# Kernel optimization log

Measured on AMD Instinct MI355X. Metric: run time of the kernel, lower is better.

The kernel has to match this reference:

```python
import jax, jax.numpy as jnp
import numpy as np

B, S, D, H = 2, 2048, 1024, 16
HD = D // H


def setup_inputs() -> dict:
    key = jax.random.key(0)
    ks = jax.random.split(key, 6)
    std = 1.0 / np.sqrt(D)
    return {
        "hidden_states": jax.random.normal(ks[0], (B, S, D), dtype=jnp.float32),
        "attention_mask": jnp.zeros((B, 1, S, S), dtype=jnp.float32),
        "Wq": jax.random.normal(ks[1], (D, D), dtype=jnp.float32) * std,
        "bq": jnp.zeros((D,), dtype=jnp.float32),
        "Wk": jax.random.normal(ks[2], (D, D), dtype=jnp.float32) * std,
        "bk": jnp.zeros((D,), dtype=jnp.float32),
        "Wv": jax.random.normal(ks[3], (D, D), dtype=jnp.float32) * std,
        "bv": jnp.zeros((D,), dtype=jnp.float32),
        "Wo": jax.random.normal(ks[4], (D, D), dtype=jnp.float32) * std,
        "bo": jnp.zeros((D,), dtype=jnp.float32),
    }


def reference(hidden_states, attention_mask, Wq, bq, Wk, bk, Wv, bv, Wo, bo):
    scale = HD ** (-0.5)
    # torch Linear: y = x @ W^T + b
    def proj(x, W, b):
        y = jnp.einsum('bsd,ed->bse', x, W) + b
        return y.reshape(B, S, H, HD).transpose(0, 2, 1, 3)  # [B,H,S,HD]
    q = proj(hidden_states, Wq, bq)
    k = proj(hidden_states, Wk, bk)
    v = proj(hidden_states, Wv, bv)
    scores = jnp.einsum('bhqd,bhkd->bhqk', q, k) * scale + attention_mask
    attn = jax.nn.softmax(scores, axis=-1)  # dropout p=0.0 -> identity
    out = jnp.einsum('bhqk,bhkd->bhqd', attn, v)
    out = out.transpose(0, 2, 1, 3).reshape(B, S, D)
    return jnp.einsum('bsd,ed->bse', out, Wo) + bo
```

## Files before the change

### kernel.cpp

```cpp
#include <hip/hip_runtime.h>
#include <hip/hip_bf16.h>
#include <stdint.h>

#define Bb 2
#define Ss 2048
#define Dd 1024
#define Hh 16
#define HD 64

typedef __attribute__((ext_vector_type(8))) __bf16 bf16x8;
typedef __attribute__((ext_vector_type(4))) __bf16 bf16x4;
typedef __attribute__((ext_vector_type(2))) __bf16 bf16x2;
typedef __attribute__((ext_vector_type(4))) float f32x4;
typedef __attribute__((ext_vector_type(16))) float f32x16;

#define LOG2E 1.44269504088896f
#define SCL2 (0.125f * LOG2E)

#define HS_N   (Bb * Ss * Dd)
#define W_N    (Dd * Dd)
#define B_N    (Dd)
#define CAN_HS 0
#define CAN_WQ (CAN_HS + HS_N)
#define CAN_BQ (CAN_WQ + W_N)
#define CAN_WK (CAN_BQ + B_N)
#define CAN_BK (CAN_WK + W_N)
#define CAN_WV (CAN_BK + B_N)
#define CAN_BV (CAN_WV + W_N)
#define CAN_WO (CAN_BV + B_N)
#define CAN_BO (CAN_WO + W_N)
#define CAN_END (CAN_BO + B_N)
#define TSZ    (Bb * Hh * Ss * HD)
#define WS_ELEMS (CAN_END + 4 * TSZ)
#define WS_NEED ((size_t)WS_ELEMS * 2)

__device__ __forceinline__ void gl_lds16(const __bf16* g, __bf16* l) {
  __builtin_amdgcn_global_load_lds(
      (const __attribute__((address_space(1))) void*)g,
      (__attribute__((address_space(3))) void*)l,
      16, 0, 0);
}

__device__ __forceinline__ void gl_lds16f(const float* g, float* l) {
  __builtin_amdgcn_global_load_lds(
      (const __attribute__((address_space(1))) void*)g,
      (__attribute__((address_space(3))) void*)l,
      16, 0, 0);
}

__device__ __forceinline__ void cfence() { asm volatile("" ::: "memory"); }

__global__ void canon_kernel(const float* hs, const float* Wq, const float* bq,
                             const float* Wk, const float* bk, const float* Wv,
                             const float* bv, const float* Wo, const float* bo,
                             __bf16* __restrict__ dst) {
  const float* srcs[9] = {hs, Wq, bq, Wk, bk, Wv, bv, Wo, bo};
  const long starts[10] = {CAN_HS, CAN_WQ, CAN_BQ, CAN_WK, CAN_BK,
                           CAN_WV, CAN_BV, CAN_WO, CAN_BO, CAN_END};
  const long nchunks = CAN_END / 8;
  for (long c = blockIdx.x * blockDim.x + threadIdx.x; c < nchunks;
       c += (long)gridDim.x * blockDim.x) {
    const long i = c * 8;
    int seg = 0;
#pragma unroll
    for (int t = 1; t < 9; t++) seg += (i >= starts[t]) ? 1 : 0;
    const float* s = srcs[seg] + (i - starts[seg]);
    bf16x8 v;
#pragma unroll
    for (int e = 0; e < 8; e++) v[e] = (__bf16)s[e];
    *(bf16x8*)(dst + i) = v;
  }
}

template <int MODE, typename OutT>
__global__ __launch_bounds__(256, 2) void gemm_bt(
    const __bf16* __restrict__ A,
    const __bf16* __restrict__ W0, const __bf16* __restrict__ W1,
    const __bf16* __restrict__ W2,
    const __bf16* __restrict__ b0, const __bf16* __restrict__ b1,
    const __bf16* __restrict__ b2,
    OutT* __restrict__ O0, OutT* __restrict__ O1, OutT* __restrict__ O2) {
  __shared__ __align__(16) __bf16 sA[128 * 32 + 12544];
  __shared__ __align__(16) __bf16 sB[128 * 32];
  const int tid = threadIdx.x;
  const int lane = tid & 63;
  const int wid = tid >> 6;
  const int quad = lane >> 4;
  const int l15 = lane & 15;
  const int mBlock = blockIdx.x * 128;

  const __bf16* W;
  const __bf16* bias;
  OutT* Out;
  int nBlock, which = 0;
  if (MODE == 0) {
    which = blockIdx.y >> 3;
    nBlock = (blockIdx.y & 7) * 128;
    W = which == 0 ? W0 : (which == 1 ? W1 : W2);
    bias = which == 0 ? b0 : (which == 1 ? b1 : b2);
    Out = which == 0 ? O0 : (which == 1 ? O1 : O2);
  } else {
    nBlock = blockIdx.y * 128;
    W = W0;
    bias = b0;
    Out = O0;
  }

  const int waveM = (wid >> 1) * 64;
  const int waveN = (wid & 1) * 64;

  f32x4 acc[4][4] = {};

  const int c1 = wid * 64 + lane;
  const int c2 = c1 + 256;
  const __bf16* Ar1 = A + (mBlock + (c1 >> 2)) * Dd + (c1 & 3) * 8;
  const __bf16* Ar2 = A + (mBlock + (c2 >> 2)) * Dd + (c2 & 3) * 8;
  const __bf16* Wr1 = W + (nBlock + (c1 >> 2)) * Dd + (c1 & 3) * 8;
  const __bf16* Wr2 = W + (nBlock + (c2 >> 2)) * Dd + (c2 & 3) * 8;
  __bf16* ldsA1 = sA + (wid * 64) * 8;
  __bf16* ldsA2 = sA + (wid * 64 + 256) * 8;
  __bf16* ldsB1 = sB + (wid * 64) * 8;
  __bf16* ldsB2 = sB + (wid * 64 + 256) * 8;

  for (int k0 = 0; k0 < Dd; k0 += 32) {
    gl_lds16(Ar1 + k0, ldsA1);
    gl_lds16(Ar2 + k0, ldsA2);
    gl_lds16(Wr1 + k0, ldsB1);
    gl_lds16(Wr2 + k0, ldsB2);
    __syncthreads();

    bf16x8 aF[4], bF[4];
#pragma unroll
    for (int mi = 0; mi < 4; mi++)
      aF[mi] = *(const bf16x8*)(sA + (waveM + mi * 16 + l15) * 32 + quad * 8);
#pragma unroll
    for (int ni = 0; ni < 4; ni++)
      bF[ni] = *(const bf16x8*)(sB + (waveN + ni * 16 + l15) * 32 + quad * 8);
#pragma unroll
    for (int mi = 0; mi < 4; mi++)
#pragma unroll
      for (int ni = 0; ni < 4; ni++)
        acc[mi][ni] = __builtin_amdgcn_mfma_f32_16x16x32_bf16(
            aF[mi], bF[ni], acc[mi][ni], 0, 0, 0);
    __syncthreads();
  }

#pragma unroll
  for (int ni = 0; ni < 4; ni++) {
    const int ng = nBlock + waveN + ni * 16 + l15;
    const float bv = (float)bias[ng];
#pragma unroll
    for (int mi = 0; mi < 4; mi++) {
      const int mg0 = mBlock + waveM + mi * 16 + quad * 4;
      if (MODE == 0 && which == 2) {
        const int b = mg0 >> 11, s0 = mg0 & 2047;
        const int h = ng >> 6, hd = ng & 63;
        bf16x4 pk;
#pragma unroll
        for (int r = 0; r < 4; r++) pk[r] = (__bf16)(acc[mi][ni][r] + bv);
        *(bf16x4*)((__bf16*)Out + (((b * Hh + h) * HD + hd) * Ss) + s0) = pk;
      } else {
#pragma unroll
        for (int r = 0; r < 4; r++) {
          float v = acc[mi][ni][r] + bv;
          const int m = mg0 + r;
          if (MODE == 0) {
            if (which == 0) v *= SCL2;
            const int b = m >> 11, s = m & 2047;
            const int h = ng >> 6, hd = ng & 63;
            Out[(((b * Hh + h) * Ss + s) * HD) + hd] = (OutT)v;
          } else {
            Out[m * Dd + ng] = (OutT)v;
          }
        }
      }
    }
  }
}

__global__ __launch_bounds__(256, 3) void attn_fused(
    const __bf16* __restrict__ Qg, const __bf16* __restrict__ Kg,
    const __bf16* __restrict__ Vt, const float* __restrict__ Mf,
    __bf16* __restrict__ Og) {
  __shared__ __align__(16) union {
    struct {
      __bf16 kv[2][8192];
      float mk[64 * 64];
    } s;
    struct {
      float O[2][64][32];
      float L[2][32];
    } m;
  } sh;

  const int tid = threadIdx.x;
  const int lane = tid & 63;
  const int wid = tid >> 6;
  const int qg = wid & 1;
  const int kvh = wid >> 1;
  const int l31 = lane & 31;
  const int hi = lane >> 5;
  const int bh = blockIdx.y;
  const int b = bh >> 4;
  const int h = bh & 15;
  const int qb0 = blockIdx.x * 64;
  const int qw = qb0 + qg * 32 + l31;

  const __bf16* Qp = Qg + (size_t)bh * Ss * HD;
  const __bf16* Kp = Kg + (size_t)bh * Ss * HD;
  const __bf16* Vp = Vt + (size_t)bh * HD * Ss;
  const float* Mp = Mf + (size_t)b * Ss * Ss;

  bf16x8 qf[4];
#pragma unroll
  for (int k = 0; k < 4; k++)
    qf[k] = *(const bf16x8*)(Qp + (size_t)qw * HD + k * 16 + hi * 8);

  const int cA = tid, cB = 256 + tid;
#define STAGE_KV(BI, KVS)                                                     \
  {                                                                           \
    const int rwA = (cA & 255) >> 2, rwB = (cB & 255) >> 2;                   \
    const int slA = (cA & 3) ^ ((rwA >> 1) & 3);                              \
    const int slB = (cB & 3) ^ ((rwB >> 1) & 3);                              \
    __bf16* kb = sh.s.kv[BI];                                                 \
    gl_lds16(Kp + ((KVS) + rwA) * HD + (cA >> 8) * 32 + slA * 8, kb + cA * 8);\
    gl_lds16(Kp + ((KVS) + rwB) * HD + (cB >> 8) * 32 + slB * 8, kb + cB * 8);\
    __bf16* vb = sh.s.kv[BI] + 4096;                                          \
    gl_lds16(Vp + (size_t)rwA * Ss + (KVS) + (cA >> 8) * 32 + slA * 8,        \
             vb + cA * 8);                                                    \
    gl_lds16(Vp + (size_t)rwB * Ss + (KVS) + (cB >> 8) * 32 + slB * 8,        \
             vb + cB * 8);                                                    \
  }

#define STAGE_M(KVS)                                                          \
  {                                                                           \
    _Pragma("unroll")                                                         \
    for (int rr = 0; rr < 4; rr++) {                                          \
      const int c = tid + rr * 256;                                           \
      const int mq = c >> 4;                                                  \
      const int kvi = ((c & 15) ^ (mq & 7)) * 4;                              \
      gl_lds16f(Mp + (size_t)(qb0 + mq) * Ss + (KVS) + kvi,                   \
                sh.s.mk + c * 4);                                             \
    }                                                                         \
  }

  f32x16 o[2] = {};
  f32x4 lacc = {0.f, 0.f, 0.f, 0.f};

  const int rsw = (l31 >> 1) & 3;

  STAGE_KV(0, 0);
  STAGE_M(0);

  for (int it = 0; it < 32; ++it) {
    const int bufc = it & 1;
    cfence();
    asm volatile("s_waitcnt vmcnt(0)" ::: "memory");
    cfence();
    __builtin_amdgcn_s_barrier();
    cfence();
    if (it < 31) {
      STAGE_KV(bufc ^ 1, (it + 1) * 64);
      cfence();
    }

    f32x4 mc[4];
    const int mq = qg * 32 + l31;
#pragma unroll
    for (int g = 0; g < 4; g++) {
      const int p16 = (8 * kvh + 2 * g + hi) ^ (l31 & 7);
      mc[g] = *(const f32x4*)(sh.s.mk + mq * 64 + p16 * 4);
    }
    cfence();
    asm volatile("s_waitcnt lgkmcnt(0)" ::: "memory");
    cfence();
    __builtin_amdgcn_s_barrier();
    cfence();
    if (it < 31) {
      STAGE_M((it + 1) * 64);
      cfence();
    }

    f32x16 sacc;
#pragma unroll
    for (int g = 0; g < 4; g++)
#pragma unroll
      for (int r = 0; r < 4; r++) sacc[g * 4 + r] = mc[g][r] * LOG2E;
    __builtin_amdgcn_s_setprio(1);
#pragma unroll
    for (int k = 0; k < 4; k++) {
      const int ps = (((k & 1) << 1) | hi) ^ rsw;
      bf16x8 kf = *(const bf16x8*)(sh.s.kv[bufc] +
                                   ((k >> 1) * 64 + kvh * 32 + l31) * 32 +
                                   ps * 8);
      sacc = __builtin_amdgcn_mfma_f32_32x32x16_bf16(kf, qf[k], sacc, 0, 0, 0);
    }
    __builtin_amdgcn_s_setprio(0);

    f32x4 sv[4];
#pragma unroll
    for (int g = 0; g < 4; g++)
#pragma unroll
      for (int r = 0; r < 4; r++)
        sv[g][r] = __builtin_amdgcn_exp2f(sacc[g * 4 + r]);
    lacc += (sv[0] + sv[1]) + (sv[2] + sv[3]);

    bf16x4 pk[4];
#pragma unroll
    for (int g = 0; g < 4; g++)
#pragma unroll
      for (int r = 0; r < 4; r++) pk[g][r] = (__bf16)sv[g][r];
    union pu { bf16x4 v; uint32_t w[2]; };
    pu s0, s1, r0, r1;
    s0.v = hi ? pk[0] : pk[1];
    s1.v = hi ? pk[2] : pk[3];
    r0.w[0] = __shfl_xor((int)s0.w[0], 32);
    r0.w[1] = __shfl_xor((int)s0.w[1], 32);
    r1.w[0] = __shfl_xor((int)s1.w[0], 32);
    r1.w[1] = __shfl_xor((int)s1.w[1], 32);
    bf16x8 pf[2];
    {
      bf16x4 lo0 = hi ? r0.v : pk[0], hi0 = hi ? pk[1] : r0.v;
      bf16x4 lo1 = hi ? r1.v : pk[2], hi1 = hi ? pk[3] : r1.v;
#pragma unroll
      for (int e = 0; e < 4; e++) {
        pf[0][e] = lo0[e]; pf[0][e + 4] = hi0[e];
        pf[1][e] = lo1[e]; pf[1][e + 4] = hi1[e];
      }
    }

    __builtin_amdgcn_s_setprio(1);
#pragma unroll
    for (int k = 0; k < 2; k++)
#pragma unroll
      for (int hb = 0; hb < 2; hb++) {
        const int ps = ((k << 1) | hi) ^ rsw;
        bf16x8 vf = *(const bf16x8*)(sh.s.kv[bufc] + 4096 +
                                     (kvh * 64 + hb * 32 + l31) * 32 +
                                     ps * 8);
        o[hb] = __builtin_amdgcn_mfma_f32_32x32x16_bf16(vf, pf[k], o[hb],
                                                        0, 0, 0);
      }
    __builtin_amdgcn_s_setprio(0);
  }

  float l = lacc[0] + lacc[1] + lacc[2] + lacc[3];
  l += __shfl_xor(l, 32);

  __syncthreads();
  if (kvh == 1) {
#pragma unroll
    for (int hb = 0; hb < 2; hb++)
#pragma unroll
      for (int r = 0; r < 16; r++) {
        const int hd = hb * 32 + (r & 3) + 8 * (r >> 2) + 4 * hi;
        sh.m.O[qg][hd][l31] = o[hb][r];
      }
    if (hi == 0) sh.m.L[qg][l31] = l;
  }
  __syncthreads();
  if (kvh == 0) {
#pragma unroll
    for (int hb = 0; hb < 2; hb++)
#pragma unroll
      for (int r = 0; r < 16; r++) {
        const int hd = hb * 32 + (r & 3) + 8 * (r >> 2) + 4 * hi;
        o[hb][r] += sh.m.O[qg][hd][l31];
      }
    l += sh.m.L[qg][l31];
    const float inv = 1.0f / l;
    __bf16* Ow = Og + (((size_t)b * Ss + qw) * Hh + h) * HD;
#pragma unroll
    for (int hb = 0; hb < 2; hb++)
#pragma unroll
      for (int g = 0; g < 4; g++) {
        const int hd = hb * 32 + g * 8 + 4 * hi;
        bf16x2 w0, w1;
        w0[0] = (__bf16)(o[hb][g * 4 + 0] * inv);
        w0[1] = (__bf16)(o[hb][g * 4 + 1] * inv);
        w1[0] = (__bf16)(o[hb][g * 4 + 2] * inv);
        w1[1] = (__bf16)(o[hb][g * 4 + 3] * inv);
        *(bf16x2*)(Ow + hd) = w0;
        *(bf16x2*)(Ow + hd + 2) = w1;
      }
  }
}

extern "C" void kernel_launch(void* const* d_in, const int* in_sizes, int n_in,
                              void* d_out, int out_size, void* d_ws,
                              size_t ws_size, hipStream_t stream) {
  if (ws_size < WS_NEED) return;

  __bf16* ws = (__bf16*)d_ws;
  const __bf16* hsC = ws + CAN_HS;
  const __bf16* WqC = ws + CAN_WQ;
  const __bf16* bqC = ws + CAN_BQ;
  const __bf16* WkC = ws + CAN_WK;
  const __bf16* bkC = ws + CAN_BK;
  const __bf16* WvC = ws + CAN_WV;
  const __bf16* bvC = ws + CAN_BV;
  const __bf16* WoC = ws + CAN_WO;
  const __bf16* boC = ws + CAN_BO;
  __bf16* Q = ws + CAN_END;
  __bf16* K = Q + TSZ;
  __bf16* V = K + TSZ;
  __bf16* AW = V + TSZ;
  float* out = (float*)d_out;

  canon_kernel<<<2048, 256, 0, stream>>>(
      (const float*)d_in[0], (const float*)d_in[2], (const float*)d_in[3],
      (const float*)d_in[4], (const float*)d_in[5], (const float*)d_in[6],
      (const float*)d_in[7], (const float*)d_in[8], (const float*)d_in[9], ws);
  gemm_bt<0, __bf16><<<dim3(32, 24), 256, 0, stream>>>(
      hsC, WqC, WkC, WvC, bqC, bkC, bvC, Q, K, V);
  attn_fused<<<dim3(32, 32), 256, 0, stream>>>(Q, K, V, (const float*)d_in[1],
                                               AW);
  gemm_bt<1, float><<<dim3(32, 8), 256, 0, stream>>>(
      AW, WoC, WoC, WoC, boC, boC, boC, out, out, out);
}
```

Before: 236.3 us.

## Precompute bf16 log2e-scaled mask and remap attention blocks for mask reuse

```diff
diff --git a/kernel.cpp b/kernel.cpp
--- a/kernel.cpp
+++ b/kernel.cpp
@@ -20,6 +20,7 @@
 #define HS_N   (Bb * Ss * Dd)
 #define W_N    (Dd * Dd)
 #define B_N    (Dd)
+#define MS_N   ((long)Bb * Ss * Ss)
 #define CAN_HS 0
 #define CAN_WQ (CAN_HS + HS_N)
 #define CAN_BQ (CAN_WQ + W_N)
@@ -41,34 +42,39 @@
       16, 0, 0);
 }
 
-__device__ __forceinline__ void gl_lds16f(const float* g, float* l) {
-  __builtin_amdgcn_global_load_lds(
-      (const __attribute__((address_space(1))) void*)g,
-      (__attribute__((address_space(3))) void*)l,
-      16, 0, 0);
-}
-
 __device__ __forceinline__ void cfence() { asm volatile("" ::: "memory"); }
 
 __global__ void canon_kernel(const float* hs, const float* Wq, const float* bq,
                              const float* Wk, const float* bk, const float* Wv,
                              const float* bv, const float* Wo, const float* bo,
-                             __bf16* __restrict__ dst) {
+                             __bf16* __restrict__ dst,
+                             const float* __restrict__ Mf,
+                             __bf16* __restrict__ mout) {
   const float* srcs[9] = {hs, Wq, bq, Wk, bk, Wv, bv, Wo, bo};
   const long starts[10] = {CAN_HS, CAN_WQ, CAN_BQ, CAN_WK, CAN_BK,
                            CAN_WV, CAN_BV, CAN_WO, CAN_BO, CAN_END};
-  const long nchunks = CAN_END / 8;
-  for (long c = blockIdx.x * blockDim.x + threadIdx.x; c < nchunks;
+  const long nA = CAN_END / 8;
+  const long nTot = nA + MS_N / 8;
+  for (long c = blockIdx.x * blockDim.x + threadIdx.x; c < nTot;
        c += (long)gridDim.x * blockDim.x) {
-    const long i = c * 8;
-    int seg = 0;
-#pragma unroll
-    for (int t = 1; t < 9; t++) seg += (i >= starts[t]) ? 1 : 0;
-    const float* s = srcs[seg] + (i - starts[seg]);
-    bf16x8 v;
-#pragma unroll
-    for (int e = 0; e < 8; e++) v[e] = (__bf16)s[e];
-    *(bf16x8*)(dst + i) = v;
+    if (c < nA) {
+      const long i = c * 8;
+      int seg = 0;
+#pragma unroll
+      for (int t = 1; t < 9; t++) seg += (i >= starts[t]) ? 1 : 0;
+      const float* s = srcs[seg] + (i - starts[seg]);
+      bf16x8 v;
+#pragma unroll
+      for (int e = 0; e < 8; e++) v[e] = (__bf16)s[e];
+      *(bf16x8*)(dst + i) = v;
+    } else {
+      const long i = (c - nA) * 8;
+      const float* s = Mf + i;
+      bf16x8 v;
+#pragma unroll
+      for (int e = 0; e < 8; e++) v[e] = (__bf16)(s[e] * LOG2E);
+      *(bf16x8*)(mout + i) = v;
+    }
   }
 }
 
@@ -178,14 +184,14 @@
   }
 }
 
-__global__ __launch_bounds__(256, 3) void attn_fused(
+__global__ __launch_bounds__(256, 4) void attn_fused(
     const __bf16* __restrict__ Qg, const __bf16* __restrict__ Kg,
-    const __bf16* __restrict__ Vt, const float* __restrict__ Mf,
+    const __bf16* __restrict__ Vt, const __bf16* __restrict__ Mbf,
     __bf16* __restrict__ Og) {
   __shared__ __align__(16) union {
     struct {
       __bf16 kv[2][8192];
-      float mk[64 * 64];
+      __bf16 mk[4096];
     } s;
     struct {
       float O[2][64][32];
@@ -200,16 +206,19 @@
   const int kvh = wid >> 1;
   const int l31 = lane & 31;
   const int hi = lane >> 5;
-  const int bh = blockIdx.y;
+
+  const int id = blockIdx.x;
+  const int j = id >> 3;
+  const int bh = (id & 7) + 8 * (j >> 5);
+  const int qb0 = (j & 31) * 64;
   const int b = bh >> 4;
   const int h = bh & 15;
-  const int qb0 = blockIdx.x * 64;
   const int qw = qb0 + qg * 32 + l31;
 
   const __bf16* Qp = Qg + (size_t)bh * Ss * HD;
   const __bf16* Kp = Kg + (size_t)bh * Ss * HD;
   const __bf16* Vp = Vt + (size_t)bh * HD * Ss;
-  const float* Mp = Mf + (size_t)b * Ss * Ss;
+  const __bf16* Mb = Mbf + (size_t)b * Ss * Ss;
 
   bf16x8 qf[4];
 #pragma unroll
@@ -235,12 +244,12 @@
 #define STAGE_M(KVS)                                                          \
   {                                                                           \
     _Pragma("unroll")                                                         \
-    for (int rr = 0; rr < 4; rr++) {                                          \
+    for (int rr = 0; rr < 2; rr++) {                                          \
       const int c = tid + rr * 256;                                           \
-      const int mq = c >> 4;                                                  \
-      const int kvi = ((c & 15) ^ (mq & 7)) * 4;                              \
-      gl_lds16f(Mp + (size_t)(qb0 + mq) * Ss + (KVS) + kvi,                   \
-                sh.s.mk + c * 4);                                             \
+      const int mq = c >> 3;                                                  \
+      const int l8 = (c & 7) ^ (mq & 7);                                      \
+      gl_lds16(Mb + (size_t)(qb0 + mq) * Ss + (KVS) + l8 * 8,                 \
+               sh.s.mk + c * 8);                                              \
     }                                                                         \
   }
 
@@ -264,12 +273,12 @@
       cfence();
     }
 
-    f32x4 mc[4];
+    bf16x4 mcv[4];
     const int mq = qg * 32 + l31;
 #pragma unroll
     for (int g = 0; g < 4; g++) {
-      const int p16 = (8 * kvh + 2 * g + hi) ^ (l31 & 7);
-      mc[g] = *(const f32x4*)(sh.s.mk + mq * 64 + p16 * 4);
+      const int p8 = (4 * kvh + g) ^ (l31 & 7);
+      mcv[g] = *(const bf16x4*)(sh.s.mk + mq * 64 + p8 * 8 + 4 * hi);
     }
     cfence();
     asm volatile("s_waitcnt lgkmcnt(0)" ::: "memory");
@@ -285,7 +294,7 @@
 #pragma unroll
     for (int g = 0; g < 4; g++)
 #pragma unroll
-      for (int r = 0; r < 4; r++) sacc[g * 4 + r] = mc[g][r] * LOG2E;
+      for (int r = 0; r < 4; r++) sacc[g * 4 + r] = (float)mcv[g][r];
     __builtin_amdgcn_s_setprio(1);
 #pragma unroll
     for (int k = 0; k < 4; k++) {
@@ -406,15 +415,16 @@
   __bf16* V = K + TSZ;
   __bf16* AW = V + TSZ;
   float* out = (float*)d_out;
+  __bf16* Mbf = (__bf16*)d_out;
 
   canon_kernel<<<2048, 256, 0, stream>>>(
       (const float*)d_in[0], (const float*)d_in[2], (const float*)d_in[3],
       (const float*)d_in[4], (const float*)d_in[5], (const float*)d_in[6],
-      (const float*)d_in[7], (const float*)d_in[8], (const float*)d_in[9], ws);
+      (const float*)d_in[7], (const float*)d_in[8], (const float*)d_in[9], ws,
+      (const float*)d_in[1], Mbf);
   gemm_bt<0, __bf16><<<dim3(32, 24), 256, 0, stream>>>(
       hsC, WqC, WkC, WvC, bqC, bkC, bvC, Q, K, V);
-  attn_fused<<<dim3(32, 32), 256, 0, stream>>>(Q, K, V, (const float*)d_in[1],
-                                               AW);
+  attn_fused<<<dim3(1024), 256, 0, stream>>>(Q, K, V, Mbf, AW);
   gemm_bt<1, float><<<dim3(32, 8), 256, 0, stream>>>(
       AW, WoC, WoC, WoC, boC, boC, boC, out, out, out);
 }
```

Result: no change. 231.9 us (-1.9%).
